# Performance work log

Hardware: AMD Instinct MI355X
Metric: run time of the kernel (lower is better)

The kernel has to match this reference:

```python
import jax, jax.numpy as jnp
import numpy as np

INTENT_DIM = 64
HIDDEN_DIM = 128
B = 16384
M = 32


def setup_inputs() -> dict:
    key = jax.random.key(0)
    ks = jax.random.split(key, 12)
    d_in = INTENT_DIM + 4
    s = lambda n: 1.0 / np.sqrt(n)
    return {
        "ego_z": jax.random.normal(ks[0], (B, INTENT_DIM), jnp.float32),
        "neighbor_zs": jax.random.normal(ks[1], (B, M, INTENT_DIM), jnp.float32),
        "neighbor_rel_pos": jax.random.normal(ks[2], (B, M, 4), jnp.float32),
        "mask": jax.random.randint(ks[3], (B, M), 0, 2, jnp.int32),
        "Wq": jax.random.uniform(ks[4], (INTENT_DIM, HIDDEN_DIM), jnp.float32, -s(INTENT_DIM), s(INTENT_DIM)),
        "bq": jnp.zeros((HIDDEN_DIM,), jnp.float32),
        "Wk": jax.random.uniform(ks[5], (d_in, HIDDEN_DIM), jnp.float32, -s(d_in), s(d_in)),
        "bk": jnp.zeros((HIDDEN_DIM,), jnp.float32),
        "Wv": jax.random.uniform(ks[6], (d_in, HIDDEN_DIM), jnp.float32, -s(d_in), s(d_in)),
        "bv": jnp.zeros((HIDDEN_DIM,), jnp.float32),
        "Wo": jax.random.uniform(ks[7], (HIDDEN_DIM, INTENT_DIM), jnp.float32, -s(HIDDEN_DIM), s(HIDDEN_DIM)),
        "bo": jnp.zeros((INTENT_DIM,), jnp.float32),
    }


def reference(ego_z, neighbor_zs, neighbor_rel_pos, mask,
              Wq, bq, Wk, bk, Wv, bv, Wo, bo):
    # concat neighbor intent + relative position: (B, M, intent+4)
    feats = jnp.concatenate([neighbor_zs, neighbor_rel_pos], axis=-1)
    q = ego_z @ Wq + bq                       # (B, H)
    k = feats @ Wk + bk                       # (B, M, H)
    v = feats @ Wv + bv                       # (B, M, H)
    scores = jnp.einsum("bh,bmh->bm", q, k) / jnp.sqrt(jnp.float32(HIDDEN_DIM))
    scores = jnp.where(mask == 0, jnp.float32(-1e9), scores)
    weights = jax.nn.softmax(scores, axis=-1)  # (B, M)
    ctx = jnp.einsum("bm,bmh->bh", weights, v)  # (B, H)
    return ctx @ Wo + bo                        # (B, intent)
```

## Files before the change

### kernel.cpp

```cpp
#include <hip/hip_runtime.h>
#include <math.h>

#define M       32
#define IDIM    64
#define DIN     68
#define HDIM    128

#define WS_A4     0
#define WS_WVO4   4352
#define WS_U0     8704
#define WS_G      8772
#define WS_C0     8836
#define WS_OUTB   8840
#define WS_FLOATS 8904

#define CST_FLOATS 8704
#define CST_WVO    4352

__global__ __launch_bounds__(256)
void ga_precompute(const float* __restrict__ Wq, const float* __restrict__ bq,
                   const float* __restrict__ Wk, const float* __restrict__ bk,
                   const float* __restrict__ Wv, const float* __restrict__ bv,
                   const float* __restrict__ Wo, const float* __restrict__ bo,
                   float* __restrict__ ws) {
  int t = blockIdx.x * 256 + threadIdx.x;
  const float4* Wq4 = (const float4*)Wq;
  const float4* Wk4 = (const float4*)Wk;
  if (t < 4352) {
    int k = t & 3, rem = t >> 2;
    int d = rem % DIN, i4 = rem / DIN;
    int i = i4 * 4 + k;
    float acc = 0.f;
    #pragma unroll 8
    for (int h4 = 0; h4 < 32; ++h4) {
      float4 a = Wq4[i*32+h4], b = Wk4[d*32+h4];
      acc = fmaf(a.x, b.x, acc); acc = fmaf(a.y, b.y, acc);
      acc = fmaf(a.z, b.z, acc); acc = fmaf(a.w, b.w, acc);
    }
    ws[WS_A4 + t] = acc;
  } else if (t < 8704) {
    int e = t - WS_WVO4;
    int k = e & 3, rem = e >> 2;
    int j = rem & 63, d4 = rem >> 6;
    int d = d4 * 4 + k;
    float acc = 0.f;
    #pragma unroll 8
    for (int h = 0; h < HDIM; ++h) acc = fmaf(Wv[d*HDIM+h], Wo[h*IDIM+j], acc);
    ws[WS_WVO4 + e] = acc;
  } else if (t < 8772) {
    int d = t - WS_U0;
    float acc = 0.f;
    for (int h = 0; h < HDIM; ++h) acc = fmaf(Wk[d*HDIM+h], bq[h], acc);
    ws[WS_U0 + d] = acc;
  } else if (t < 8836) {
    int i = t - WS_G;
    float acc = 0.f;
    for (int h = 0; h < HDIM; ++h) acc = fmaf(Wq[i*HDIM+h], bk[h], acc);
    ws[WS_G + i] = acc;
  } else if (t == 8836) {
    float acc = 0.f;
    for (int h = 0; h < HDIM; ++h) acc = fmaf(bq[h], bk[h], acc);
    ws[WS_C0] = acc;
  } else if (t < WS_FLOATS) {
    int j = t - WS_OUTB;
    float acc = bo[j];
    for (int h = 0; h < HDIM; ++h) acc = fmaf(bv[h], Wo[h*IDIM+j], acc);
    ws[WS_OUTB + j] = acc;
  }
}

template <int CTRL>
__device__ __forceinline__ float dpp_add(float x) {
  int t = __builtin_amdgcn_update_dpp(0, __float_as_int(x), CTRL, 0xF, 0xF, true);
  return x + __int_as_float(t);
}
__device__ __forceinline__ float red16(float x) {
  x = dpp_add<0xB1>(x);
  x = dpp_add<0x4E>(x);
  x = dpp_add<0x124>(x);
  x = dpp_add<0x128>(x);
  return x;
}

__global__ __launch_bounds__(512, 2)
void ga_main(const float* __restrict__ ego,
             const float* __restrict__ nz,
             const float* __restrict__ rp,
             const int*   __restrict__ mask,
             const float* __restrict__ ws,
             float* __restrict__ out) {
  __shared__ float cst   [CST_FLOATS];
  __shared__ float u_lds [8 * 64];
  __shared__ float w_lds [8 * 32];
  __shared__ float fb_lds[8 * 64];

  const int tid  = threadIdx.x;
  const int wave = tid >> 6;
  const int lane = tid & 63;
  const int t4   = lane >> 4;
  const int l    = lane & 15;
  const int row  = __builtin_amdgcn_readfirstlane(blockIdx.x * 8 + wave);

  #define GLL(K) do { int c = wave + 8*(K); if (c < 34)                         \
    __builtin_amdgcn_global_load_lds(                                           \
      (const __attribute__((address_space(1))) void*)(ws + c*256 + lane*4),     \
      (__attribute__((address_space(3))) void*)(cst + c*256), 16, 0, 0); } while(0)
  GLL(0); GLL(1); GLL(2); GLL(3); GLL(4);
  #undef GLL
  __builtin_amdgcn_sched_barrier(0);

  const float4* zsrc4 = (const float4*)(nz + (size_t)row * (M * IDIM));
  float4 z0 = zsrc4[0*64 + lane], z1 = zsrc4[1*64 + lane];
  float4 z2 = zsrc4[2*64 + lane], z3 = zsrc4[3*64 + lane];
  float4 z4 = zsrc4[4*64 + lane], z5 = zsrc4[5*64 + lane];
  float4 z6 = zsrc4[6*64 + lane], z7 = zsrc4[7*64 + lane];
  const float4* rpsrc = (const float4*)(rp + (size_t)row * (M * 4));
  const float4 rpa = rpsrc[4 * (lane & 7) + t4];
  const float4 rpb = rpsrc[lane & 31];
  const int    mreg = mask[row * M + (lane & 31)];

  __builtin_amdgcn_sched_barrier(0);
  asm volatile("s_waitcnt vmcnt(11)" ::: "memory");
  __builtin_amdgcn_s_barrier();
  asm volatile("" ::: "memory");

  const float* egoR = ego + (size_t)row * IDIM;
  {
    float ua0 = 0.f, ua1 = 0.f, ua2 = 0.f, ua3 = 0.f;
    #pragma unroll 8
    for (int i4 = 0; i4 < 16; ++i4) {
      const float4 av = *(const float4*)&cst[(i4 * DIN + lane) << 2];
      ua0 = fmaf(egoR[i4 * 4],     av.x, ua0);
      ua1 = fmaf(egoR[i4 * 4 + 1], av.y, ua1);
      ua2 = fmaf(egoR[i4 * 4 + 2], av.z, ua2);
      ua3 = fmaf(egoR[i4 * 4 + 3], av.w, ua3);
    }
    u_lds[wave * 64 + lane] = ((ua0 + ua1) + (ua2 + ua3)) + ws[WS_U0 + lane];
  }
  float uh0, uh1, uh2, uh3;
  {
    const float4 av = *(const float4*)&cst[(l * DIN + IDIM + t4) << 2];
    float pt = egoR[l * 4] * av.x;
    pt = fmaf(egoR[l * 4 + 1], av.y, pt);
    pt = fmaf(egoR[l * 4 + 2], av.z, pt);
    pt = fmaf(egoR[l * 4 + 3], av.w, pt);
    pt = red16(pt);
    int pti = __float_as_int(pt);
    uh0 = __int_as_float(__builtin_amdgcn_readlane(pti, 0))  + ws[WS_U0 + 64];
    uh1 = __int_as_float(__builtin_amdgcn_readlane(pti, 16)) + ws[WS_U0 + 65];
    uh2 = __int_as_float(__builtin_amdgcn_readlane(pti, 32)) + ws[WS_U0 + 66];
    uh3 = __int_as_float(__builtin_amdgcn_readlane(pti, 48)) + ws[WS_U0 + 67];
  }
  float cterm;
  {
    float pc = egoR[lane] * ws[WS_G + lane];
    pc = red16(pc);
    pc += __shfl_xor(pc, 16);
    pc += __shfl_xor(pc, 32);
    cterm = pc + ws[WS_C0];
  }

  asm volatile("" ::: "memory");

  const float4 u4 = *(const float4*)&u_lds[wave * 64 + l * 4];
  const float rpdot = fmaf(rpa.w, uh3, fmaf(rpa.z, uh2,
                      fmaf(rpa.y, uh1, rpa.x * uh0)));
  const unsigned int mbits  = (unsigned int)__ballot(mreg != 0);
  const unsigned int mshift = mbits >> t4;

  #define SC(IT, Z) float s##IT; {                                        \
    float p = (Z).x * u4.x;                                               \
    p = fmaf((Z).y, u4.y, p);                                             \
    p = fmaf((Z).z, u4.z, p);                                             \
    p = fmaf((Z).w, u4.w, p);                                             \
    p += (l == (IT)) ? rpdot : 0.f;                                       \
    p = red16(p);                                                         \
    s##IT = ((mshift >> (4*(IT))) & 1u)                                   \
          ? (p + cterm) * 0.088388347648318447f : -1e9f; }
  SC(0, z0) SC(1, z1) SC(2, z2) SC(3, z3)
  SC(4, z4) SC(5, z5) SC(6, z6) SC(7, z7)
  #undef SC

  float mx = fmaxf(fmaxf(fmaxf(s0, s1), fmaxf(s2, s3)),
                   fmaxf(fmaxf(s4, s5), fmaxf(s6, s7)));
  mx = fmaxf(mx, __shfl_xor(mx, 16));
  mx = fmaxf(mx, __shfl_xor(mx, 32));
  float e0 = __expf(s0 - mx), e1 = __expf(s1 - mx);
  float e2 = __expf(s2 - mx), e3 = __expf(s3 - mx);
  float e4 = __expf(s4 - mx), e5 = __expf(s5 - mx);
  float e6 = __expf(s6 - mx), e7 = __expf(s7 - mx);
  float se = ((e0 + e1) + (e2 + e3)) + ((e4 + e5) + (e6 + e7));
  se += __shfl_xor(se, 16);
  se += __shfl_xor(se, 32);
  const float rse = __builtin_amdgcn_rcpf(se);
  const float w0 = e0 * rse, w1 = e1 * rse, w2 = e2 * rse, w3 = e3 * rse;
  const float w4 = e4 * rse, w5 = e5 * rse, w6 = e6 * rse, w7 = e7 * rse;

  float p40 = 0.f, p41 = 0.f, p42 = 0.f, p43 = 0.f;
  #define FB(W, Z) do {                                                   \
    p40 = fmaf((W), (Z).x, p40);                                          \
    p41 = fmaf((W), (Z).y, p41);                                          \
    p42 = fmaf((W), (Z).z, p42);                                          \
    p43 = fmaf((W), (Z).w, p43);                                          \
  } while (0);
  FB(w0, z0) FB(w1, z1) FB(w2, z2) FB(w3, z3)
  FB(w4, z4) FB(w5, z5) FB(w6, z6) FB(w7, z7)
  #undef FB
  p40 += __shfl_xor(p40, 16);  p40 += __shfl_xor(p40, 32);
  p41 += __shfl_xor(p41, 16);  p41 += __shfl_xor(p41, 32);
  p42 += __shfl_xor(p42, 16);  p42 += __shfl_xor(p42, 32);
  p43 += __shfl_xor(p43, 16);  p43 += __shfl_xor(p43, 32);

  if (l == 0) {
    float4 wa; wa.x = w0; wa.y = w1; wa.z = w2; wa.w = w3;
    float4 wb; wb.x = w4; wb.y = w5; wb.z = w6; wb.w = w7;
    *(float4*)&w_lds[wave * 32 + t4 * 8]     = wa;
    *(float4*)&w_lds[wave * 32 + t4 * 8 + 4] = wb;
  }
  if (lane < 16) {
    float4 fv; fv.x = p40; fv.y = p41; fv.z = p42; fv.w = p43;
    *(float4*)&fb_lds[wave * 64 + l * 4] = fv;
  }
  asm volatile("" ::: "memory");

  const int mm = lane & 31;
  const float wm = w_lds[wave * 32 + (mm & 3) * 8 + (mm >> 2)];
  float pr0 = wm * rpb.x, pr1 = wm * rpb.y, pr2 = wm * rpb.z, pr3 = wm * rpb.w;
  pr0 = red16(pr0); pr0 += __shfl_xor(pr0, 16);
  pr1 = red16(pr1); pr1 += __shfl_xor(pr1, 16);
  pr2 = red16(pr2); pr2 += __shfl_xor(pr2, 16);
  pr3 = red16(pr3); pr3 += __shfl_xor(pr3, 16);

  float oa0 = 0.f, oa1 = 0.f, oa2 = 0.f, oa3 = 0.f;
  #pragma unroll 8
  for (int d4 = 0; d4 < 16; ++d4) {
    const float4 wv = *(const float4*)&cst[CST_WVO + ((d4 * IDIM + lane) << 2)];
    const float4 fv = *(const float4*)&fb_lds[wave * 64 + d4 * 4];
    oa0 = fmaf(fv.x, wv.x, oa0);
    oa1 = fmaf(fv.y, wv.y, oa1);
    oa2 = fmaf(fv.z, wv.z, oa2);
    oa3 = fmaf(fv.w, wv.w, oa3);
  }
  {
    const float4 wv = *(const float4*)&cst[CST_WVO + ((16 * IDIM + lane) << 2)];
    oa0 = fmaf(pr0, wv.x, oa0);
    oa1 = fmaf(pr1, wv.y, oa1);
    oa2 = fmaf(pr2, wv.z, oa2);
    oa3 = fmaf(pr3, wv.w, oa3);
  }
  out[(size_t)row * IDIM + lane] = ((oa0 + oa1) + (oa2 + oa3)) + ws[WS_OUTB + lane];
}

extern "C" void kernel_launch(void* const* d_in, const int* in_sizes, int n_in,
                              void* d_out, int out_size, void* d_ws, size_t ws_size,
                              hipStream_t stream) {
  const float* ego = (const float*)d_in[0];
  const float* nz  = (const float*)d_in[1];
  const float* rp  = (const float*)d_in[2];
  const int*   mk  = (const int*)d_in[3];
  const float* Wq  = (const float*)d_in[4];
  const float* bq  = (const float*)d_in[5];
  const float* Wk  = (const float*)d_in[6];
  const float* bk  = (const float*)d_in[7];
  const float* Wv  = (const float*)d_in[8];
  const float* bv  = (const float*)d_in[9];
  const float* Wo  = (const float*)d_in[10];
  const float* bo  = (const float*)d_in[11];
  float* ws = (float*)d_ws;
  float* o  = (float*)d_out;

  const int nrows = in_sizes[0] / IDIM;

  ga_precompute<<<(WS_FLOATS + 255) / 256, 256, 0, stream>>>(
      Wq, bq, Wk, bk, Wv, bv, Wo, bo, ws);
  ga_main<<<nrows / 8, 512, 0, stream>>>(ego, nz, rp, mk, ws, o);
}
```

Before: 41.29 us.

## Split precompute dot products across 4 lanes and drop redundant rel-pos load

The weight-folding precompute kernel now gives each output four threads that each cover a quarter of the hidden dimension and combine their partials with DPP. This shortens the serial per-thread loops and raises parallelism in the small kernel. In the main kernel, the second rel-pos load and the LDS staging of attention weights are removed; each lane instead selects its weight from registers, reuses the rpa registers and halves the result to correct for duplicated coverage. The launch-bounds occupancy hint rises from 2 to 4 blocks, which may constrain register allocation and add spills.

```diff
diff --git a/kernel.cpp b/kernel.cpp
--- a/kernel.cpp
+++ b/kernel.cpp
@@ -17,6 +17,32 @@
 #define CST_FLOATS 8704
 #define CST_WVO    4352
 
+template <int CTRL>
+__device__ __forceinline__ float dpp_add(float x) {
+  int t = __builtin_amdgcn_update_dpp(0, __float_as_int(x), CTRL, 0xF, 0xF, true);
+  return x + __int_as_float(t);
+}
+__device__ __forceinline__ float red4(float x) {
+  x = dpp_add<0xB1>(x);
+  x = dpp_add<0x4E>(x);
+  return x;
+}
+__device__ __forceinline__ float red16(float x) {
+  x = dpp_add<0xB1>(x);
+  x = dpp_add<0x4E>(x);
+  x = dpp_add<0x124>(x);
+  x = dpp_add<0x128>(x);
+  return x;
+}
+
+#define SEG_A   0
+#define SEG_W   17408
+#define SEG_U0  34816
+#define SEG_G   35088
+#define SEG_OB  35344
+#define SEG_C0  35600
+#define PRE_T   35601
+
 __global__ __launch_bounds__(256)
 void ga_precompute(const float* __restrict__ Wq, const float* __restrict__ bq,
                    const float* __restrict__ Wk, const float* __restrict__ bk,
@@ -24,65 +50,89 @@
                    const float* __restrict__ Wo, const float* __restrict__ bo,
                    float* __restrict__ ws) {
   int t = blockIdx.x * 256 + threadIdx.x;
+  if (t >= PRE_T) return;
   const float4* Wq4 = (const float4*)Wq;
   const float4* Wk4 = (const float4*)Wk;
-  if (t < 4352) {
-    int k = t & 3, rem = t >> 2;
+  const float4* Wv4 = (const float4*)Wv;
+  const float4* bq4 = (const float4*)bq;
+  const float4* bk4 = (const float4*)bk;
+  const int sub = t & 3;
+  const int h4b = sub * 8;
+
+  if (t < SEG_W) {
+    int e = t >> 2;
+    int k = e & 3, rem = e >> 2;
     int d = rem % DIN, i4 = rem / DIN;
     int i = i4 * 4 + k;
     float acc = 0.f;
-    #pragma unroll 8
-    for (int h4 = 0; h4 < 32; ++h4) {
-      float4 a = Wq4[i*32+h4], b = Wk4[d*32+h4];
+    #pragma unroll
+    for (int hh = 0; hh < 8; ++hh) {
+      float4 a = Wq4[i*32 + h4b + hh], b = Wk4[d*32 + h4b + hh];
       acc = fmaf(a.x, b.x, acc); acc = fmaf(a.y, b.y, acc);
       acc = fmaf(a.z, b.z, acc); acc = fmaf(a.w, b.w, acc);
     }
-    ws[WS_A4 + t] = acc;
-  } else if (t < 8704) {
-    int e = t - WS_WVO4;
+    acc = red4(acc);
+    if (sub == 0) ws[WS_A4 + e] = acc;
+  } else if (t < SEG_U0) {
+    int e = (t - SEG_W) >> 2;
     int k = e & 3, rem = e >> 2;
     int j = rem & 63, d4 = rem >> 6;
     int d = d4 * 4 + k;
     float acc = 0.f;
-    #pragma unroll 8
-    for (int h = 0; h < HDIM; ++h) acc = fmaf(Wv[d*HDIM+h], Wo[h*IDIM+j], acc);
-    ws[WS_WVO4 + e] = acc;
-  } else if (t < 8772) {
-    int d = t - WS_U0;
-    float acc = 0.f;
-    for (int h = 0; h < HDIM; ++h) acc = fmaf(Wk[d*HDIM+h], bq[h], acc);
-    ws[WS_U0 + d] = acc;
-  } else if (t < 8836) {
-    int i = t - WS_G;
-    float acc = 0.f;
-    for (int h = 0; h < HDIM; ++h) acc = fmaf(Wq[i*HDIM+h], bk[h], acc);
-    ws[WS_G + i] = acc;
-  } else if (t == 8836) {
+    #pragma unroll
+    for (int hh = 0; hh < 8; ++hh) {
+      float4 v = Wv4[d*32 + h4b + hh];
+      int h = (h4b + hh) * 4;
+      acc = fmaf(v.x, Wo[(h    )*IDIM + j], acc);
+      acc = fmaf(v.y, Wo[(h + 1)*IDIM + j], acc);
+      acc = fmaf(v.z, Wo[(h + 2)*IDIM + j], acc);
+      acc = fmaf(v.w, Wo[(h + 3)*IDIM + j], acc);
+    }
+    acc = red4(acc);
+    if (sub == 0) ws[WS_WVO4 + e] = acc;
+  } else if (t < SEG_G) {
+    int d = (t - SEG_U0) >> 2;
+    float acc = 0.f;
+    #pragma unroll
+    for (int hh = 0; hh < 8; ++hh) {
+      float4 a = Wk4[d*32 + h4b + hh], b = bq4[h4b + hh];
+      acc = fmaf(a.x, b.x, acc); acc = fmaf(a.y, b.y, acc);
+      acc = fmaf(a.z, b.z, acc); acc = fmaf(a.w, b.w, acc);
+    }
+    acc = red4(acc);
+    if (sub == 0) ws[WS_U0 + d] = acc;
+  } else if (t < SEG_OB) {
+    int i = (t - SEG_G) >> 2;
+    float acc = 0.f;
+    #pragma unroll
+    for (int hh = 0; hh < 8; ++hh) {
+      float4 a = Wq4[i*32 + h4b + hh], b = bk4[h4b + hh];
+      acc = fmaf(a.x, b.x, acc); acc = fmaf(a.y, b.y, acc);
+      acc = fmaf(a.z, b.z, acc); acc = fmaf(a.w, b.w, acc);
+    }
+    acc = red4(acc);
+    if (sub == 0) ws[WS_G + i] = acc;
+  } else if (t < SEG_C0) {
+    int j = (t - SEG_OB) >> 2;
+    float acc = 0.f;
+    #pragma unroll
+    for (int hh = 0; hh < 8; ++hh) {
+      int h = (h4b + hh) * 4;
+      acc = fmaf(bv[h    ], Wo[(h    )*IDIM + j], acc);
+      acc = fmaf(bv[h + 1], Wo[(h + 1)*IDIM + j], acc);
+      acc = fmaf(bv[h + 2], Wo[(h + 2)*IDIM + j], acc);
+      acc = fmaf(bv[h + 3], Wo[(h + 3)*IDIM + j], acc);
+    }
+    acc = red4(acc);
+    if (sub == 0) ws[WS_OUTB + j] = acc + bo[j];
+  } else {
     float acc = 0.f;
     for (int h = 0; h < HDIM; ++h) acc = fmaf(bq[h], bk[h], acc);
     ws[WS_C0] = acc;
-  } else if (t < WS_FLOATS) {
-    int j = t - WS_OUTB;
-    float acc = bo[j];
-    for (int h = 0; h < HDIM; ++h) acc = fmaf(bv[h], Wo[h*IDIM+j], acc);
-    ws[WS_OUTB + j] = acc;
-  }
-}
-
-template <int CTRL>
-__device__ __forceinline__ float dpp_add(float x) {
-  int t = __builtin_amdgcn_update_dpp(0, __float_as_int(x), CTRL, 0xF, 0xF, true);
-  return x + __int_as_float(t);
-}
-__device__ __forceinline__ float red16(float x) {
-  x = dpp_add<0xB1>(x);
-  x = dpp_add<0x4E>(x);
-  x = dpp_add<0x124>(x);
-  x = dpp_add<0x128>(x);
-  return x;
-}
-
-__global__ __launch_bounds__(512, 2)
+  }
+}
+
+__global__ __launch_bounds__(512, 4)
 void ga_main(const float* __restrict__ ego,
              const float* __restrict__ nz,
              const float* __restrict__ rp,
@@ -91,7 +141,6 @@
              float* __restrict__ out) {
   __shared__ float cst   [CST_FLOATS];
   __shared__ float u_lds [8 * 64];
-  __shared__ float w_lds [8 * 32];
   __shared__ float fb_lds[8 * 64];
 
   const int tid  = threadIdx.x;
@@ -116,11 +165,10 @@
   float4 z6 = zsrc4[6*64 + lane], z7 = zsrc4[7*64 + lane];
   const float4* rpsrc = (const float4*)(rp + (size_t)row * (M * 4));
   const float4 rpa = rpsrc[4 * (lane & 7) + t4];
-  const float4 rpb = rpsrc[lane & 31];
   const int    mreg = mask[row * M + (lane & 31)];
 
   __builtin_amdgcn_sched_barrier(0);
-  asm volatile("s_waitcnt vmcnt(11)" ::: "memory");
+  asm volatile("s_waitcnt vmcnt(10)" ::: "memory");
   __builtin_amdgcn_s_barrier();
   asm volatile("" ::: "memory");
 
@@ -137,7 +185,7 @@
     }
     u_lds[wave * 64 + lane] = ((ua0 + ua1) + (ua2 + ua3)) + ws[WS_U0 + lane];
   }
-  float uh0, uh1, uh2, uh3;
+  float rpdot;
   {
     const float4 av = *(const float4*)&cst[(l * DIN + IDIM + t4) << 2];
     float pt = egoR[l * 4] * av.x;
@@ -146,10 +194,11 @@
     pt = fmaf(egoR[l * 4 + 3], av.w, pt);
     pt = red16(pt);
     int pti = __float_as_int(pt);
-    uh0 = __int_as_float(__builtin_amdgcn_readlane(pti, 0))  + ws[WS_U0 + 64];
-    uh1 = __int_as_float(__builtin_amdgcn_readlane(pti, 16)) + ws[WS_U0 + 65];
-    uh2 = __int_as_float(__builtin_amdgcn_readlane(pti, 32)) + ws[WS_U0 + 66];
-    uh3 = __int_as_float(__builtin_amdgcn_readlane(pti, 48)) + ws[WS_U0 + 67];
+    float uh0 = __int_as_float(__builtin_amdgcn_readlane(pti, 0))  + ws[WS_U0 + 64];
+    float uh1 = __int_as_float(__builtin_amdgcn_readlane(pti, 16)) + ws[WS_U0 + 65];
+    float uh2 = __int_as_float(__builtin_amdgcn_readlane(pti, 32)) + ws[WS_U0 + 66];
+    float uh3 = __int_as_float(__builtin_amdgcn_readlane(pti, 48)) + ws[WS_U0 + 67];
+    rpdot = fmaf(rpa.w, uh3, fmaf(rpa.z, uh2, fmaf(rpa.y, uh1, rpa.x * uh0)));
   }
   float cterm;
   {
@@ -163,8 +212,6 @@
   asm volatile("" ::: "memory");
 
   const float4 u4 = *(const float4*)&u_lds[wave * 64 + l * 4];
-  const float rpdot = fmaf(rpa.w, uh3, fmaf(rpa.z, uh2,
-                      fmaf(rpa.y, uh1, rpa.x * uh0)));
   const unsigned int mbits  = (unsigned int)__ballot(mreg != 0);
   const unsigned int mshift = mbits >> t4;
 
@@ -210,26 +257,26 @@
   p41 += __shfl_xor(p41, 16);  p41 += __shfl_xor(p41, 32);
   p42 += __shfl_xor(p42, 16);  p42 += __shfl_xor(p42, 32);
   p43 += __shfl_xor(p43, 16);  p43 += __shfl_xor(p43, 32);
-
-  if (l == 0) {
-    float4 wa; wa.x = w0; wa.y = w1; wa.z = w2; wa.w = w3;
-    float4 wb; wb.x = w4; wb.y = w5; wb.z = w6; wb.w = w7;
-    *(float4*)&w_lds[wave * 32 + t4 * 8]     = wa;
-    *(float4*)&w_lds[wave * 32 + t4 * 8 + 4] = wb;
-  }
   if (lane < 16) {
     float4 fv; fv.x = p40; fv.y = p41; fv.z = p42; fv.w = p43;
     *(float4*)&fb_lds[wave * 64 + l * 4] = fv;
   }
+
+  float wsel;
+  {
+    float a0 = (l & 1) ? w1 : w0, a1 = (l & 1) ? w3 : w2;
+    float a2 = (l & 1) ? w5 : w4, a3 = (l & 1) ? w7 : w6;
+    float b0 = (l & 2) ? a1 : a0, b1 = (l & 2) ? a3 : a2;
+    wsel = 0.5f * ((l & 4) ? b1 : b0);
+  }
+  float pr0 = wsel * rpa.x, pr1 = wsel * rpa.y;
+  float pr2 = wsel * rpa.z, pr3 = wsel * rpa.w;
+  pr0 = red16(pr0); pr0 += __shfl_xor(pr0, 16); pr0 += __shfl_xor(pr0, 32);
+  pr1 = red16(pr1); pr1 += __shfl_xor(pr1, 16); pr1 += __shfl_xor(pr1, 32);
+  pr2 = red16(pr2); pr2 += __shfl_xor(pr2, 16); pr2 += __shfl_xor(pr2, 32);
+  pr3 = red16(pr3); pr3 += __shfl_xor(pr3, 16); pr3 += __shfl_xor(pr3, 32);
+
   asm volatile("" ::: "memory");
-
-  const int mm = lane & 31;
-  const float wm = w_lds[wave * 32 + (mm & 3) * 8 + (mm >> 2)];
-  float pr0 = wm * rpb.x, pr1 = wm * rpb.y, pr2 = wm * rpb.z, pr3 = wm * rpb.w;
-  pr0 = red16(pr0); pr0 += __shfl_xor(pr0, 16);
-  pr1 = red16(pr1); pr1 += __shfl_xor(pr1, 16);
-  pr2 = red16(pr2); pr2 += __shfl_xor(pr2, 16);
-  pr3 = red16(pr3); pr3 += __shfl_xor(pr3, 16);
 
   float oa0 = 0.f, oa1 = 0.f, oa2 = 0.f, oa3 = 0.f;
   #pragma unroll 8
@@ -271,7 +318,7 @@
 
   const int nrows = in_sizes[0] / IDIM;
 
-  ga_precompute<<<(WS_FLOATS + 255) / 256, 256, 0, stream>>>(
+  ga_precompute<<<(PRE_T + 255) / 256, 256, 0, stream>>>(
       Wq, bq, Wk, bk, Wv, bv, Wo, bo, ws);
   ga_main<<<nrows / 8, 512, 0, stream>>>(ego, nz, rp, mk, ws, o);
 }
```

Result: faster. 38.24 us, median of 3 (-7.4%).
